# Optimization experiments

Measured on AMD Instinct MI355X. Metric: run time of the kernel, lower is better.

## Reference

```python
import jax, jax.numpy as jnp
import numpy as np

NTA = 65536   # total atoms across all crystals
NC = 1024     # number of crystals
NO = 256      # descriptor output dim (desc.NO)
H = 332       # int(NO * 1.3) hidden dim of per-species MLP
S = 4         # number of species


def setup_inputs() -> dict:
    key = jax.random.key(0)
    ks = jax.random.split(key, 8)
    symbols = jax.random.randint(ks[0], (NTA,), 0, S)
    positions = jax.random.normal(ks[1], (NTA, 3), jnp.float32) * 3.0
    cells = jax.random.normal(ks[2], (NC, 3, 3), jnp.float32)
    pbcs = jnp.ones((NC, 3), dtype=bool)
    energyidx = jnp.arange(NC)
    crystalidx = jax.random.randint(ks[3], (NTA,), 0, NC)
    # stand-in descriptor projection (replaces external REANN desc module)
    Wd = jax.random.normal(ks[4], (3, NO), jnp.float32) * 0.5
    # stacked per-species MLP params: Linear(NO,H) -> SiLU -> Linear(H,1)
    W1 = jax.random.normal(ks[5], (S, NO, H), jnp.float32) / np.sqrt(NO).astype(np.float32)
    b1 = jnp.zeros((S, H), jnp.float32)
    W2 = jax.random.normal(ks[6], (S, H), jnp.float32) / np.sqrt(H).astype(np.float32)
    b2 = jnp.zeros((S,), jnp.float32)
    return {
        "symbols": symbols, "positions": positions, "cells": cells,
        "pbcs": pbcs, "energyidx": energyidx, "crystalidx": crystalidx,
        "Wd": Wd, "W1": W1, "b1": b1, "W2": W2, "b2": b2,
    }


def _atomic_energies(positions, symbols, Wd, W1, b1, W2, b2):
    # stand-in descriptor: [NTA, NO]
    feat = jnp.tanh(positions @ Wd)
    n_species = W1.shape[0]
    e = jnp.zeros((positions.shape[0],), feat.dtype)
    # species-routed small MLPs: dense compute + select (fixed small loop over species)
    for s in range(n_species):
        h = jax.nn.silu(feat @ W1[s] + b1[s])       # [NTA, H]
        es = h @ W2[s] + b2[s]                      # [NTA]
        e = jnp.where(symbols == s, es, e)
    return e


def reference(symbols, positions, cells, pbcs, energyidx, crystalidx, Wd, W1, b1, W2, b2):
    num_crystals = energyidx.shape[0]

    def total_energy(pos):
        en = _atomic_energies(pos, symbols, Wd, W1, b1, W2, b2)   # [NTA]
        E = jax.ops.segment_sum(en, crystalidx, num_segments=num_crystals)  # [NC]
        return jnp.sum(E), (en, E)

    # torch code: forces = grad(sum(energy), positions)  (positive gradient)
    forces, (energies, energy) = jax.grad(total_energy, has_aux=True)(positions)
    return (energies, energy, forces)
```

## Files before the change

kernel.cpp:

```cpp
#include <hip/hip_runtime.h>

#define NTA 65536
#define NC 1024
#define NO 256
#define HDIM 332
#define HP 352
#define NSP 4
#define NOUT (NTA + NC + NTA*3)
#define SORT_CAP (NTA + 4*128)

#define DP_STRIDE 720
#define LDS_MAIN  159744

typedef __attribute__((ext_vector_type(8))) short short8;
typedef __attribute__((ext_vector_type(4))) float f32x4;

#define OFF_CNT   0
#define OFF_CUR   64
#define OFF_START 128
#define OFF_FLAG  160
#define OFF_SORT  256
#define OFF_B1P   264448
#define OFF_W2P   270080
#define OFF_W1T   275712
#define OFF_W1P   996608

__device__ __forceinline__ unsigned short f2bf(float f){
  unsigned int u = __builtin_bit_cast(unsigned int, f);
  u += 0x7fffu + ((u>>16)&1u);
  return (unsigned short)(u>>16);
}
__device__ __forceinline__ float bf2f(unsigned short h){
  unsigned int u = ((unsigned int)h)<<16;
  return __builtin_bit_cast(float, u);
}
__device__ __forceinline__ float ldf(const void* p, int idx, int isbf){
  if (isbf) return bf2f(((const unsigned short*)p)[idx]);
  return ((const float*)p)[idx];
}
__device__ __forceinline__ float rcpf(float x){ return __builtin_amdgcn_rcpf(x); }

__global__ void k_init2(const int* __restrict__ sym, unsigned int* __restrict__ cnt,
                        int* __restrict__ sorted, const unsigned short* __restrict__ posu,
                        unsigned int* __restrict__ flag, float* __restrict__ dout){
  __shared__ unsigned int h[NSP];
  int t = threadIdx.x;
  if (t < NSP) h[t] = 0u;
  __syncthreads();
  int i = blockIdx.x*256 + t;
  if (i < SORT_CAP) sorted[i] = -1;
  if (i < NC) dout[NTA + i] = 0.f;
  if (i < NTA) atomicAdd(&h[sym[i]], 1u);
  __syncthreads();
  if (t < NSP && h[t]) atomicAdd(&cnt[t], h[t]);
  if (blockIdx.x == 257 && t < 64){
    unsigned short u = posu[2*t];
    int e = (u>>7)&0xFF;
    bool inr = (e >= 110 && e <= 140);
    unsigned long long m = __ballot(inr);
    if (t == 0) flag[0] = (__popcll(m) >= 32) ? 1u : 0u;
  }
}

__global__ void k_scatter2(const int* __restrict__ sym, const unsigned int* __restrict__ cnt,
                           unsigned int* __restrict__ cur, int* __restrict__ sorted,
                           int* __restrict__ gstarts){
  __shared__ int sl[NSP+1];
  int t = threadIdx.x;
  if (t == 0){
    int a = 0; sl[0] = 0;
    #pragma unroll
    for (int s=0;s<NSP;s++){ a += (int)(((cnt[s]+127u)>>7)<<7); sl[s+1] = a; }
    if (blockIdx.x == 0){
      #pragma unroll
      for (int s=0;s<=NSP;s++) gstarts[s] = sl[s];
    }
  }
  __syncthreads();
  int i = blockIdx.x*256 + t;
  int s = sym[i];
  int lane = t & 63;
  #pragma unroll
  for (int ss=0; ss<NSP; ss++){
    unsigned long long m = __ballot(s==ss);
    if (s == ss){
      int leader = __builtin_ctzll(m);
      int cw = __popcll(m);
      unsigned int b = 0;
      if (lane == leader) b = atomicAdd(&cur[ss], (unsigned int)cw);
      b = (unsigned int)__shfl((int)b, leader);
      int rank = __popcll(m & ((1ull<<lane) - 1ull));
      sorted[sl[ss] + (int)b + rank] = i;
    }
  }
}

__global__ void k_prepw2(const void* __restrict__ W1, const void* __restrict__ b1,
                         const void* __restrict__ W2, const unsigned int* __restrict__ flag,
                         unsigned short* __restrict__ w1t, unsigned short* __restrict__ w1p,
                         float* __restrict__ b1p, float* __restrict__ w2p){
  __shared__ unsigned short T[32][36];
  const int isbf = (int)flag[0];
  const int bid = blockIdx.x;
  const int s  = bid / 88;
  const int jt = (bid % 88) / 8;
  const int it = bid % 8;
  const int t = threadIdx.x;
  {
    const int il = t >> 3;
    const int j4 = (t & 7) * 4;
    const int i = it*32 + il;
    #pragma unroll
    for (int e=0;e<4;e++){
      int j = jt*32 + j4 + e;
      float v = (j < HDIM) ? ldf(W1, (s*NO + i)*HDIM + j, isbf) : 0.f;
      T[il][j4+e] = f2bf(v);
    }
  }
  __syncthreads();
  {
    const int jl = t >> 3;
    const int i4 = (t & 7) * 4;
    ushort4 v; v.x = T[i4][jl]; v.y = T[i4+1][jl]; v.z = T[i4+2][jl]; v.w = T[i4+3][jl];
    *(ushort4*)&w1t[(s*HP + jt*32 + jl)*NO + it*32 + i4] = v;
    const int il = t >> 3;
    const int j4 = (t & 7) * 4;
    ushort4 u; u.x = T[il][j4]; u.y = T[il][j4+1]; u.z = T[il][j4+2]; u.w = T[il][j4+3];
    *(ushort4*)&w1p[(s*NO + it*32 + il)*HP + jt*32 + j4] = u;
  }
  if (it == 0 && t < 32){
    int j = jt*32 + t;
    b1p[s*HP + j] = (j < HDIM) ? ldf(b1, s*HDIM + j, isbf) : 0.f;
    w2p[s*HP + j] = (j < HDIM) ? ldf(W2, s*HDIM + j, isbf) : 0.f;
  }
}

__global__ __launch_bounds__(512,2) void k_main(
    const int* __restrict__ sorted, const int* __restrict__ starts,
    const void* __restrict__ pos, const void* __restrict__ Wd,
    const unsigned short* __restrict__ W1T, const unsigned short* __restrict__ W1P,
    const float* __restrict__ b1p, const float* __restrict__ w2p,
    const void* __restrict__ b2g, const int* __restrict__ crys,
    const unsigned int* __restrict__ flag, float* __restrict__ dout)
{
  extern __shared__ char smem[];
  ushort4* wdT = (ushort4*)smem;
  char* featB  = smem + 2048;
  char* dpB    = smem + 2048 + 65536;
  float* Epart = (float*)dpB;
  float* Fpart = (float*)(dpB + 4096);

  const int base = blockIdx.x*128;
  if (base >= starts[4]) return;
  const int isbf = (int)flag[0];
  int sp = 0;
  #pragma unroll
  for (int s=1;s<NSP;s++) sp = (base >= starts[s]) ? s : sp;

  const int tid = threadIdx.x;
  const int l = tid & 63;
  const int w = tid >> 6;
  const int c = l & 15;
  const int g = l >> 4;

  if (tid < 256){
    float x = ldf(Wd, tid, isbf), y = ldf(Wd, NO+tid, isbf), z = ldf(Wd, 2*NO+tid, isbf);
    ushort4 u; u.x = f2bf(x); u.y = f2bf(y); u.z = f2bf(z); u.w = 0;
    wdT[tid] = u;
  }
  __syncthreads();

  {
    const int m = tid & 127;
    const int h = tid >> 7;
    int a = sorted[base + m];
    float px=0.f, py=0.f, pz=0.f;
    if (a >= 0){ px = ldf(pos,3*a,isbf); py = ldf(pos,3*a+1,isbf); pz = ldf(pos,3*a+2,isbf); }
    const int swz = (m&7)<<4;
    char* rowp = featB + m*512;
    #pragma unroll
    for (int k8=0;k8<8;k8++){
      int i0 = h*64 + k8*8;
      unsigned int pk[4];
      #pragma unroll
      for (int p2=0;p2<4;p2++){
        unsigned short hv[2];
        #pragma unroll
        for (int e2=0;e2<2;e2++){
          ushort4 wv = wdT[i0 + 2*p2 + e2];
          float v = px*bf2f(wv.x) + py*bf2f(wv.y) + pz*bf2f(wv.z);
          float e = __expf(2.f*v);
          hv[e2] = f2bf(1.f - 2.f*rcpf(e+1.f));
        }
        pk[p2] = (unsigned int)hv[0] | ((unsigned int)hv[1]<<16);
      }
      *(uint4*)(rowp + ((i0*2) ^ swz)) = make_uint4(pk[0],pk[1],pk[2],pk[3]);
    }
  }
  __syncthreads();

  const unsigned short* W1Ts = W1T + sp*HP*NO;
  const int fr0 = (w<6) ? w*3 : 18 + (w-6)*2;
  const int nT  = (w<6) ? 3 : 2;
  f32x4 acc[3][8];
  #pragma unroll
  for (int t=0;t<3;t++)
    #pragma unroll
    for (int nb=0;nb<8;nb++) acc[t][nb] = f32x4{0.f,0.f,0.f,0.f};

  short8 pf[3];
  #pragma unroll
  for (int t=0;t<3;t++)
    if (t < nT) pf[t] = *(const short8*)((const char*)W1Ts + ((fr0+t)*16 + c)*512 + g*16);

  #pragma unroll
  for (int kk=0; kk<8; kk++){
    short8 cur[3];
    #pragma unroll
    for (int t=0;t<3;t++) cur[t] = pf[t];
    if (kk < 7){
      #pragma unroll
      for (int t=0;t<3;t++)
        if (t < nT) pf[t] = *(const short8*)((const char*)W1Ts + ((fr0+t)*16 + c)*512 + (kk+1)*64 + g*16);
    }
    short8 bfr[8];
    #pragma unroll
    for (int nb=0;nb<8;nb++){
      int m = nb*16 + c;
      bfr[nb] = *(const short8*)(featB + m*512 + ((kk*64 + g*16) ^ ((m&7)<<4)));
    }
    #pragma unroll
    for (int t=0;t<3;t++){
      if (t < nT){
        #pragma unroll
        for (int nb=0;nb<8;nb++)
          acc[t][nb] = __builtin_amdgcn_mfma_f32_16x16x32_bf16(cur[t], bfr[nb], acc[t][nb], 0,0,0);
      }
    }
  }

  const float* b1s = b1p + sp*HP;
  const float* w2s = w2p + sp*HP;
  float esp[8] = {0.f,0.f,0.f,0.f,0.f,0.f,0.f,0.f};
  #pragma unroll
  for (int t=0;t<3;t++){
    if (t < nT){
      const int j0 = (fr0+t)*16 + g*4;
      const float4 b1v = *(const float4*)(b1s + j0);
      const float4 w2v = *(const float4*)(w2s + j0);
      const float* b1a = (const float*)&b1v;
      const float* w2a = (const float*)&w2v;
      #pragma unroll
      for (int nb=0;nb<8;nb++){
        const int m = nb*16 + c;
        unsigned short dph[4];
        #pragma unroll
        for (int q=0;q<4;q++){
          float pre = acc[t][nb][q] + b1a[q];
          float sg = rcpf(1.f + __expf(-pre));
          float h = pre*sg;
          esp[nb] += h*w2a[q];
          float dsl = sg*(1.f + pre*(1.f - sg));
          dph[q] = f2bf(w2a[q]*dsl);
        }
        *(uint2*)(dpB + m*DP_STRIDE + j0*2) =
            make_uint2((unsigned)dph[0] | ((unsigned)dph[1]<<16),
                       (unsigned)dph[2] | ((unsigned)dph[3]<<16));
      }
    }
  }
  float e8[8];
  #pragma unroll
  for (int nb=0;nb<8;nb++){
    float e = esp[nb];
    e += __shfl_xor(e, 16);
    e += __shfl_xor(e, 32);
    e8[nb] = e;
  }
  __syncthreads();

  const unsigned short* W1Ps = W1P + sp*NO*HP;
  f32x4 acc2[2][8];
  #pragma unroll
  for (int t2=0;t2<2;t2++)
    #pragma unroll
    for (int nb=0;nb<8;nb++) acc2[t2][nb] = f32x4{0.f,0.f,0.f,0.f};

  short8 pf2[2];
  #pragma unroll
  for (int t2=0;t2<2;t2++)
    pf2[t2] = *(const short8*)((const char*)W1Ps + ((2*w+t2)*16 + c)*704 + g*16);

  #pragma unroll
  for (int kk=0; kk<11; kk++){
    short8 cur2[2];
    #pragma unroll
    for (int t2=0;t2<2;t2++) cur2[t2] = pf2[t2];
    if (kk < 10){
      #pragma unroll
      for (int t2=0;t2<2;t2++)
        pf2[t2] = *(const short8*)((const char*)W1Ps + ((2*w+t2)*16 + c)*704 + (kk+1)*64 + g*16);
    }
    short8 bfr[8];
    #pragma unroll
    for (int nb=0;nb<8;nb++){
      int m = nb*16 + c;
      bfr[nb] = *(const short8*)(dpB + m*DP_STRIDE + kk*64 + g*16);
    }
    #pragma unroll
    for (int t2=0;t2<2;t2++){
      #pragma unroll
      for (int nb=0;nb<8;nb++)
        acc2[t2][nb] = __builtin_amdgcn_mfma_f32_16x16x32_bf16(cur2[t2], bfr[nb], acc2[t2][nb], 0,0,0);
    }
  }

  float fax[8], fay[8], faz[8];
  #pragma unroll
  for (int nb=0;nb<8;nb++){ fax[nb]=0.f; fay[nb]=0.f; faz[nb]=0.f; }
  #pragma unroll
  for (int t2=0;t2<2;t2++){
    const int i0 = (2*w+t2)*16 + g*4;
    #pragma unroll
    for (int nb=0;nb<8;nb++){
      const int m = nb*16 + c;
      uint2 fpk = *(const uint2*)(featB + m*512 + ((i0*2) ^ ((m&7)<<4)));
      unsigned short fh[4];
      fh[0] = (unsigned short)(fpk.x & 0xffffu); fh[1] = (unsigned short)(fpk.x >> 16);
      fh[2] = (unsigned short)(fpk.y & 0xffffu); fh[3] = (unsigned short)(fpk.y >> 16);
      #pragma unroll
      for (int q=0;q<4;q++){
        float ff = bf2f(fh[q]);
        float gsc = acc2[t2][nb][q] * (1.f - ff*ff);
        ushort4 wv = wdT[i0 + q];
        fax[nb] += gsc*bf2f(wv.x);
        fay[nb] += gsc*bf2f(wv.y);
        faz[nb] += gsc*bf2f(wv.z);
      }
    }
  }
  #pragma unroll
  for (int nb=0;nb<8;nb++){
    float x = fax[nb], y = fay[nb], z = faz[nb];
    x += __shfl_xor(x, 16); x += __shfl_xor(x, 32);
    y += __shfl_xor(y, 16); y += __shfl_xor(y, 32);
    z += __shfl_xor(z, 16); z += __shfl_xor(z, 32);
    fax[nb] = x; fay[nb] = y; faz[nb] = z;
  }
  __syncthreads();

  if (g == 0){
    #pragma unroll
    for (int nb=0;nb<8;nb++){
      const int m = nb*16 + c;
      Epart[w*128 + m] = e8[nb];
      Fpart[(w*128 + m)*3 + 0] = fax[nb];
      Fpart[(w*128 + m)*3 + 1] = fay[nb];
      Fpart[(w*128 + m)*3 + 2] = faz[nb];
    }
  }
  __syncthreads();

  if (tid < 128){
    int a = sorted[base + tid];
    if (a >= 0){
      float E = ldf(b2g, sp, isbf);
      float fx = 0.f, fy = 0.f, fz = 0.f;
      #pragma unroll
      for (int ww=0; ww<8; ww++){
        E  += Epart[ww*128 + tid];
        fx += Fpart[(ww*128 + tid)*3 + 0];
        fy += Fpart[(ww*128 + tid)*3 + 1];
        fz += Fpart[(ww*128 + tid)*3 + 2];
      }
      dout[a] = E;
      atomicAdd(&dout[NTA + crys[a]], E);
      dout[NTA + NC + 3*a + 0] = fx;
      dout[NTA + NC + 3*a + 1] = fy;
      dout[NTA + NC + 3*a + 2] = fz;
    }
  }
}

extern "C" void kernel_launch(void* const* d_in, const int* in_sizes, int n_in,
                              void* d_out, int out_size, void* d_ws, size_t ws_size,
                              hipStream_t stream) {
  const int*   symbols    = (const int*)  d_in[0];
  const void*  positions  = d_in[1];
  const int*   crystalidx = (const int*)  d_in[5];
  const void*  Wd         = d_in[6];
  const void*  W1         = d_in[7];
  const void*  b1         = d_in[8];
  const void*  W2         = d_in[9];
  const void*  b2         = d_in[10];
  float* dout = (float*)d_out;

  char* ws = (char*)d_ws;
  unsigned int* cnt    = (unsigned int*)(ws + OFF_CNT);
  unsigned int* cur    = (unsigned int*)(ws + OFF_CUR);
  int*          starts = (int*)         (ws + OFF_START);
  unsigned int* flag   = (unsigned int*)(ws + OFF_FLAG);
  int*          sorted = (int*)         (ws + OFF_SORT);
  float*        b1p    = (float*)       (ws + OFF_B1P);
  float*        w2p    = (float*)       (ws + OFF_W2P);
  unsigned short* w1t  = (unsigned short*)(ws + OFF_W1T);
  unsigned short* w1pp = (unsigned short*)(ws + OFF_W1P);

  hipFuncSetAttribute((const void*)k_main,
                      hipFuncAttributeMaxDynamicSharedMemorySize, LDS_MAIN);

  hipMemsetAsync(ws, 0, 256, stream);
  k_init2   <<<258, 256, 0, stream>>>(symbols, cnt, sorted,
                                      (const unsigned short*)positions, flag, dout);
  k_scatter2<<<256, 256, 0, stream>>>(symbols, cnt, cur, sorted, starts);
  k_prepw2  <<<352, 256, 0, stream>>>(W1, b1, W2, flag, w1t, w1pp, b1p, w2p);
  k_main    <<<516, 512, LDS_MAIN, stream>>>(sorted, starts, positions, Wd,
                                             w1t, w1pp, b1p, w2p, b2, crystalidx,
                                             flag, dout);
}
```

Baseline: 139.1 us.

## Stage W1 weight tiles through LDS with async double-buffered global_load_lds

Weight A-fragments for both GEMMs were loaded per-wave straight from global memory into registers. They are now staged into double-buffered LDS tiles with async global_load_lds, with a barrier every k-step. The LDS layout is repacked so dpB aliases the feature buffer and staging buffers, which shrinks total LDS. The backward pass now recomputes tanh features in fp32 from reloaded positions instead of reading the bf16 features from LDS, which frees the feature region for reuse. This adds per-iteration __syncthreads and extra transcendental work in the force epilogue.

```diff
diff --git a/kernel.cpp b/kernel.cpp
--- a/kernel.cpp
+++ b/kernel.cpp
@@ -9,8 +9,14 @@
 #define NOUT (NTA + NC + NTA*3)
 #define SORT_CAP (NTA + 4*128)
 
+#define LDS_FEATB 2048
+#define LDS_A1B0  67584
+#define LDS_A1B1  90112
+#define LDS_DPB   2048
+#define LDS_A2B0  94208
+#define LDS_A2B1  110592
+#define LDS_MAIN  126976
 #define DP_STRIDE 720
-#define LDS_MAIN  159744
 
 typedef __attribute__((ext_vector_type(8))) short short8;
 typedef __attribute__((ext_vector_type(4))) float f32x4;
@@ -39,6 +45,12 @@
   return ((const float*)p)[idx];
 }
 __device__ __forceinline__ float rcpf(float x){ return __builtin_amdgcn_rcpf(x); }
+
+__device__ __forceinline__ void gld16(const void* g, void* l){
+  __builtin_amdgcn_global_load_lds(
+      (const __attribute__((address_space(1))) void*)g,
+      (__attribute__((address_space(3))) void*)l, 16, 0, 0);
+}
 
 __global__ void k_init2(const int* __restrict__ sym, unsigned int* __restrict__ cnt,
                         int* __restrict__ sorted, const unsigned short* __restrict__ posu,
@@ -135,6 +147,22 @@
   }
 }
 
+#define ISSUE_A1(dstbuf, kk) do{                                               \
+    int p_ = tid;                                                              \
+    gld16(W1Tb + (p_>>2)*512 + (kk)*64 + (p_&3)*16, (dstbuf) + p_*16);         \
+    p_ = tid + 512;                                                            \
+    gld16(W1Tb + (p_>>2)*512 + (kk)*64 + (p_&3)*16, (dstbuf) + p_*16);         \
+    if (w < 6){ p_ = tid + 1024;                                               \
+      gld16(W1Tb + (p_>>2)*512 + (kk)*64 + (p_&3)*16, (dstbuf) + p_*16); }     \
+  }while(0)
+
+#define ISSUE_A2(dstbuf, kk) do{                                               \
+    int p_ = tid;                                                              \
+    gld16(W1Pb + (p_>>2)*704 + (kk)*64 + (p_&3)*16, (dstbuf) + p_*16);         \
+    p_ = tid + 512;                                                            \
+    gld16(W1Pb + (p_>>2)*704 + (kk)*64 + (p_&3)*16, (dstbuf) + p_*16);         \
+  }while(0)
+
 __global__ __launch_bounds__(512,2) void k_main(
     const int* __restrict__ sorted, const int* __restrict__ starts,
     const void* __restrict__ pos, const void* __restrict__ Wd,
@@ -145,10 +173,14 @@
 {
   extern __shared__ char smem[];
   ushort4* wdT = (ushort4*)smem;
-  char* featB  = smem + 2048;
-  char* dpB    = smem + 2048 + 65536;
-  float* Epart = (float*)dpB;
-  float* Fpart = (float*)(dpB + 4096);
+  char* featB = smem + LDS_FEATB;
+  char* a1b0  = smem + LDS_A1B0;
+  char* a1b1  = smem + LDS_A1B1;
+  char* dpB   = smem + LDS_DPB;
+  char* a2b0  = smem + LDS_A2B0;
+  char* a2b1  = smem + LDS_A2B1;
+  float* Epart = (float*)(smem + LDS_DPB);
+  float* Fpart = (float*)(smem + LDS_DPB + 4096);
 
   const int base = blockIdx.x*128;
   if (base >= starts[4]) return;
@@ -163,12 +195,20 @@
   const int c = l & 15;
   const int g = l >> 4;
 
+  const unsigned short* W1Ts = W1T + sp*HP*NO;
+  const unsigned short* W1Ps = W1P + sp*NO*HP;
+  const char* W1Tb = (const char*)W1Ts;
+  const char* W1Pb = (const char*)W1Ps;
+
   if (tid < 256){
     float x = ldf(Wd, tid, isbf), y = ldf(Wd, NO+tid, isbf), z = ldf(Wd, 2*NO+tid, isbf);
     ushort4 u; u.x = f2bf(x); u.y = f2bf(y); u.z = f2bf(z); u.w = 0;
     wdT[tid] = u;
   }
   __syncthreads();
+
+  ISSUE_A1(a1b0, 0);
+  ISSUE_A1(a1b1, 1);
 
   {
     const int m = tid & 127;
@@ -199,7 +239,6 @@
   }
   __syncthreads();
 
-  const unsigned short* W1Ts = W1T + sp*HP*NO;
   const int fr0 = (w<6) ? w*3 : 18 + (w-6)*2;
   const int nT  = (w<6) ? 3 : 2;
   f32x4 acc[3][8];
@@ -208,37 +247,33 @@
     #pragma unroll
     for (int nb=0;nb<8;nb++) acc[t][nb] = f32x4{0.f,0.f,0.f,0.f};
 
-  short8 pf[3];
-  #pragma unroll
-  for (int t=0;t<3;t++)
-    if (t < nT) pf[t] = *(const short8*)((const char*)W1Ts + ((fr0+t)*16 + c)*512 + g*16);
-
-  #pragma unroll
-  for (int kk=0; kk<8; kk++){
-    short8 cur[3];
-    #pragma unroll
-    for (int t=0;t<3;t++) cur[t] = pf[t];
-    if (kk < 7){
-      #pragma unroll
-      for (int t=0;t<3;t++)
-        if (t < nT) pf[t] = *(const short8*)((const char*)W1Ts + ((fr0+t)*16 + c)*512 + (kk+1)*64 + g*16);
-    }
+  #pragma unroll
+  for (int j=0;j<8;j++){
+    char* ab = (j&1) ? a1b1 : a1b0;
     short8 bfr[8];
     #pragma unroll
     for (int nb=0;nb<8;nb++){
       int m = nb*16 + c;
-      bfr[nb] = *(const short8*)(featB + m*512 + ((kk*64 + g*16) ^ ((m&7)<<4)));
-    }
+      bfr[nb] = *(const short8*)(featB + m*512 + ((j*64 + g*16) ^ ((m&7)<<4)));
+    }
+    short8 afr[3];
+    #pragma unroll
+    for (int t=0;t<3;t++)
+      if (t < nT) afr[t] = *(const short8*)(ab + ((fr0+t)*16 + c)*64 + g*16);
     #pragma unroll
     for (int t=0;t<3;t++){
       if (t < nT){
         #pragma unroll
         for (int nb=0;nb<8;nb++)
-          acc[t][nb] = __builtin_amdgcn_mfma_f32_16x16x32_bf16(cur[t], bfr[nb], acc[t][nb], 0,0,0);
+          acc[t][nb] = __builtin_amdgcn_mfma_f32_16x16x32_bf16(afr[t], bfr[nb], acc[t][nb], 0,0,0);
       }
     }
-  }
-
+    __syncthreads();
+    if (j < 6) ISSUE_A1(ab, j+2);
+  }
+
+  ISSUE_A2(a2b0, 0);
+  ISSUE_A2(a2b1, 1);
   const float* b1s = b1p + sp*HP;
   const float* w2s = w2p + sp*HP;
   float esp[8] = {0.f,0.f,0.f,0.f,0.f,0.f,0.f,0.f};
@@ -279,42 +314,44 @@
   }
   __syncthreads();
 
-  const unsigned short* W1Ps = W1P + sp*NO*HP;
   f32x4 acc2[2][8];
   #pragma unroll
   for (int t2=0;t2<2;t2++)
     #pragma unroll
     for (int nb=0;nb<8;nb++) acc2[t2][nb] = f32x4{0.f,0.f,0.f,0.f};
 
-  short8 pf2[2];
-  #pragma unroll
-  for (int t2=0;t2<2;t2++)
-    pf2[t2] = *(const short8*)((const char*)W1Ps + ((2*w+t2)*16 + c)*704 + g*16);
-
-  #pragma unroll
-  for (int kk=0; kk<11; kk++){
-    short8 cur2[2];
-    #pragma unroll
-    for (int t2=0;t2<2;t2++) cur2[t2] = pf2[t2];
-    if (kk < 10){
-      #pragma unroll
-      for (int t2=0;t2<2;t2++)
-        pf2[t2] = *(const short8*)((const char*)W1Ps + ((2*w+t2)*16 + c)*704 + (kk+1)*64 + g*16);
-    }
+  #pragma unroll
+  for (int j=0;j<11;j++){
+    char* ab = (j&1) ? a2b1 : a2b0;
     short8 bfr[8];
     #pragma unroll
     for (int nb=0;nb<8;nb++){
       int m = nb*16 + c;
-      bfr[nb] = *(const short8*)(dpB + m*DP_STRIDE + kk*64 + g*16);
-    }
+      bfr[nb] = *(const short8*)(dpB + m*DP_STRIDE + j*64 + g*16);
+    }
+    short8 afr2[2];
+    #pragma unroll
+    for (int t2=0;t2<2;t2++)
+      afr2[t2] = *(const short8*)(ab + ((2*w+t2)*16 + c)*64 + g*16);
     #pragma unroll
     for (int t2=0;t2<2;t2++){
       #pragma unroll
       for (int nb=0;nb<8;nb++)
-        acc2[t2][nb] = __builtin_amdgcn_mfma_f32_16x16x32_bf16(cur2[t2], bfr[nb], acc2[t2][nb], 0,0,0);
-    }
-  }
-
+        acc2[t2][nb] = __builtin_amdgcn_mfma_f32_16x16x32_bf16(afr2[t2], bfr[nb], acc2[t2][nb], 0,0,0);
+    }
+    __syncthreads();
+    if (j < 9) ISSUE_A2(ab, j+2);
+  }
+
+  int a8[8]; float px8[8], py8[8], pz8[8];
+  #pragma unroll
+  for (int nb=0;nb<8;nb++){
+    int aa = sorted[base + nb*16 + c];
+    a8[nb] = aa;
+    float x=0.f,y=0.f,z=0.f;
+    if (aa >= 0){ x=ldf(pos,3*aa,isbf); y=ldf(pos,3*aa+1,isbf); z=ldf(pos,3*aa+2,isbf); }
+    px8[nb]=x; py8[nb]=y; pz8[nb]=z;
+  }
   float fax[8], fay[8], faz[8];
   #pragma unroll
   for (int nb=0;nb<8;nb++){ fax[nb]=0.f; fay[nb]=0.f; faz[nb]=0.f; }
@@ -322,20 +359,18 @@
   for (int t2=0;t2<2;t2++){
     const int i0 = (2*w+t2)*16 + g*4;
     #pragma unroll
-    for (int nb=0;nb<8;nb++){
-      const int m = nb*16 + c;
-      uint2 fpk = *(const uint2*)(featB + m*512 + ((i0*2) ^ ((m&7)<<4)));
-      unsigned short fh[4];
-      fh[0] = (unsigned short)(fpk.x & 0xffffu); fh[1] = (unsigned short)(fpk.x >> 16);
-      fh[2] = (unsigned short)(fpk.y & 0xffffu); fh[3] = (unsigned short)(fpk.y >> 16);
-      #pragma unroll
-      for (int q=0;q<4;q++){
-        float ff = bf2f(fh[q]);
-        float gsc = acc2[t2][nb][q] * (1.f - ff*ff);
-        ushort4 wv = wdT[i0 + q];
-        fax[nb] += gsc*bf2f(wv.x);
-        fay[nb] += gsc*bf2f(wv.y);
-        faz[nb] += gsc*bf2f(wv.z);
+    for (int q=0;q<4;q++){
+      ushort4 wv = wdT[i0 + q];
+      float wx = bf2f(wv.x), wy = bf2f(wv.y), wz = bf2f(wv.z);
+      #pragma unroll
+      for (int nb=0;nb<8;nb++){
+        float v = px8[nb]*wx + py8[nb]*wy + pz8[nb]*wz;
+        float e = __expf(2.f*v);
+        float f = 1.f - 2.f*rcpf(e+1.f);
+        float gsc = acc2[t2][nb][q] * (1.f - f*f);
+        fax[nb] += gsc*wx;
+        fay[nb] += gsc*wy;
+        faz[nb] += gsc*wz;
       }
     }
   }
@@ -406,10 +441,10 @@
   unsigned short* w1t  = (unsigned short*)(ws + OFF_W1T);
   unsigned short* w1pp = (unsigned short*)(ws + OFF_W1P);
 
-  hipFuncSetAttribute((const void*)k_main,
+  (void)hipFuncSetAttribute((const void*)k_main,
                       hipFuncAttributeMaxDynamicSharedMemorySize, LDS_MAIN);
 
-  hipMemsetAsync(ws, 0, 256, stream);
+  (void)hipMemsetAsync(ws, 0, 256, stream);
   k_init2   <<<258, 256, 0, stream>>>(symbols, cnt, sorted,
                                       (const unsigned short*)positions, flag, dout);
   k_scatter2<<<256, 256, 0, stream>>>(symbols, cnt, cur, sorted, starts);
```

Result: slower. 161.3 us (+15.9%).
